# Kernel tuning notes

Hardware: AMD Instinct MI355X
Metric: run time of the kernel (lower is better)

Reference implementation:

```python
import jax, jax.numpy as jnp
import numpy as np

N_NODES = 50000
N_EDGES = 800000
F_IN, F_HID, F_OUT = 512, 64, 16


def setup_inputs() -> dict:
    key = jax.random.key(0)
    k1, k2, k3, k4, k5, k6 = jax.random.split(key, 6)
    x = jax.random.normal(k1, (N_NODES, F_IN), dtype=jnp.float32)
    edge_index = jax.random.randint(k2, (2, N_EDGES), 0, N_NODES, dtype=jnp.int64)
    # Glorot-style init for GCNConv linear weights, zero bias (PyG default)
    W1 = jax.random.normal(k3, (F_IN, F_HID), dtype=jnp.float32) * (1.0 / np.sqrt(F_IN))
    b1 = jnp.zeros((F_HID,), dtype=jnp.float32)
    W2 = jax.random.normal(k4, (F_HID, F_OUT), dtype=jnp.float32) * (1.0 / np.sqrt(F_HID))
    b2 = jnp.zeros((F_OUT,), dtype=jnp.float32)
    return {"x": x, "edge_index": edge_index, "W1": W1, "b1": b1, "W2": W2, "b2": b2}


def _gcn_conv(x, W, b, src, dst, norm, num_nodes):
    # x' = W x, then symmetric-normalized neighbor aggregation (scatter-add at dst)
    h = x @ W                                   # [N, F_out]
    msg = h[src] * norm[:, None]                # gather + scale  [E+N, F_out]
    out = jax.ops.segment_sum(msg, dst, num_segments=num_nodes)
    return out + b


def _gcn_norm(edge_index, num_nodes):
    # add self loops, compute deg^{-1/2}[src] * deg^{-1/2}[dst]
    loops = jnp.arange(num_nodes, dtype=edge_index.dtype)
    src = jnp.concatenate([edge_index[0], loops])
    dst = jnp.concatenate([edge_index[1], loops])
    deg = jax.ops.segment_sum(jnp.ones_like(dst, dtype=jnp.float32), dst,
                              num_segments=num_nodes)
    dinv = jnp.where(deg > 0, jax.lax.rsqrt(deg), 0.0)
    norm = dinv[src] * dinv[dst]                # [E+N]
    return src, dst, norm


def reference(x, edge_index, W1, b1, W2, b2):
    num_nodes = x.shape[0]
    src, dst, norm = _gcn_norm(edge_index, num_nodes)
    h = _gcn_conv(x, W1, b1, src, dst, norm, num_nodes)
    h = jax.nn.relu(h)
    return _gcn_conv(h, W2, b2, src, dst, norm, num_nodes)
```

## Files before the change

kernel.cpp:

```cpp
#include <hip/hip_runtime.h>

#define N_NODES 50000
#define N_EDGES 800000
#define F_IN    512
#define F_HID   64
#define F_OUT   16
#define NT      (N_NODES / 16)
#define GRID    512
#define CAP     64

typedef short bf16x8 __attribute__((ext_vector_type(8)));
typedef float f32x4  __attribute__((ext_vector_type(4)));

__device__ __forceinline__ short bhi_of(float v) {
    return (short)(__float_as_uint(v) >> 16);
}
__device__ __forceinline__ short blo_of(float v) {
    float hif = __uint_as_float(__float_as_uint(v) & 0xffff0000u);
    return (short)(__float_as_uint(v - hif) >> 16);
}

__global__ __launch_bounds__(512) void k_mega(const float* __restrict__ x,
                                              const float* __restrict__ W1,
                                              const int* __restrict__ src,
                                              const int* __restrict__ dst,
                                              int* __restrict__ count,
                                              int* __restrict__ padded,
                                              float* __restrict__ h) {
    for (int e = blockIdx.x * 512 + threadIdx.x; e < N_EDGES; e += GRID * 512) {
        int d = dst[e];
        int pos = atomicAdd(&count[d], 1);
        if (pos < CAP) padded[(size_t)d * CAP + pos] = src[e];
    }

    __shared__ __align__(16) float Abuf[2][8192];
    __shared__ float red[2][4][16][17];
    const int wave = threadIdx.x >> 6;
    const int lane = threadIdx.x & 63;
    const int m  = lane & 15, q = lane >> 4;
    const int kw = wave >> 2;
    const int cg = wave & 3;

    bf16x8 Bh[8], Bl[8];
#pragma unroll
    for (int s = 0; s < 8; ++s)
#pragma unroll
        for (int j = 0; j < 8; ++j) {
            float w = W1[(size_t)((kw * 8 + s) * 32 + q * 8 + j) * F_HID + cg * 16 + m];
            Bh[s][j] = bhi_of(w);
            Bl[s][j] = blo_of(w);
        }

    const int t0 = (int)(((long)NT * blockIdx.x) / GRID);
    const int t1 = (int)(((long)NT * (blockIdx.x + 1)) / GRID);

    int tile = t0;
    {
        const char* gb = (const char*)(x + (size_t)tile * 16 * F_IN);
        char* lb = (char*)&Abuf[0][0];
#pragma unroll
        for (int i = 0; i < 4; ++i) {
            const int c = wave * 4 + i;
            const int o = c * 1024 + lane * 16;
            const int sw = ((c >> 1) & 7) << 4;
            *(f32x4*)(lb + (o ^ sw)) = *(const f32x4*)(gb + o);
        }
    }
    __syncthreads();

    int p = 0;
    const int swr = (m & 7) << 4;
    while (true) {
        const int next = tile + 1;

        f32x4 v[4];
        if (next < t1) {
            const char* gb = (const char*)(x + (size_t)next * 16 * F_IN);
#pragma unroll
            for (int i = 0; i < 4; ++i) {
                const int o = (wave * 4 + i) * 1024 + lane * 16;
                v[i] = *(const f32x4*)(gb + o);
            }
        }

        f32x4 accA = {0, 0, 0, 0}, accB = {0, 0, 0, 0};
        const char* ab = (const char*)&Abuf[p][0];
#pragma unroll
        for (int s = 0; s < 8; ++s) {
            const int abase = m * 2048 + kw * 1024 + s * 128 + q * 32;
            f32x4 x0 = *(const f32x4*)(ab + (abase ^ swr));
            f32x4 x1 = *(const f32x4*)(ab + ((abase + 16) ^ swr));
            bf16x8 ahi, alo;
#pragma unroll
            for (int j = 0; j < 4; ++j) {
                ahi[j] = bhi_of(x0[j]);  alo[j] = blo_of(x0[j]);
                ahi[j + 4] = bhi_of(x1[j]);  alo[j + 4] = blo_of(x1[j]);
            }
            if (s & 1) {
                accB = __builtin_amdgcn_mfma_f32_16x16x32_bf16(ahi, Bh[s], accB, 0, 0, 0);
                accB = __builtin_amdgcn_mfma_f32_16x16x32_bf16(alo, Bh[s], accB, 0, 0, 0);
                accB = __builtin_amdgcn_mfma_f32_16x16x32_bf16(ahi, Bl[s], accB, 0, 0, 0);
            } else {
                accA = __builtin_amdgcn_mfma_f32_16x16x32_bf16(ahi, Bh[s], accA, 0, 0, 0);
                accA = __builtin_amdgcn_mfma_f32_16x16x32_bf16(alo, Bh[s], accA, 0, 0, 0);
                accA = __builtin_amdgcn_mfma_f32_16x16x32_bf16(ahi, Bl[s], accA, 0, 0, 0);
            }
        }
        f32x4 acc = accA + accB;

        if (next < t1) {
            char* lb = (char*)&Abuf[p ^ 1][0];
#pragma unroll
            for (int i = 0; i < 4; ++i) {
                const int c = wave * 4 + i;
                const int o = c * 1024 + lane * 16;
                const int sw = ((c >> 1) & 7) << 4;
                *(f32x4*)(lb + (o ^ sw)) = v[i];
            }
        }

        if (kw == 1) {
#pragma unroll
            for (int r = 0; r < 4; ++r)
                red[p][cg][q * 4 + r][m] = acc[r];
        }
        __syncthreads();

        if (kw == 0) {
            const int r0 = tile * 16;
#pragma unroll
            for (int r = 0; r < 4; ++r)
                h[(size_t)(r0 + q * 4 + r) * F_HID + cg * 16 + m] =
                    acc[r] + red[p][cg][q * 4 + r][m];
        }
        if (next >= t1) break;
        tile = next;
        p ^= 1;
    }
}

__global__ __launch_bounds__(256) void k_agg64f(const int* __restrict__ count,
                                                const int* __restrict__ padded,
                                                const float* __restrict__ h,
                                                const float* __restrict__ b1,
                                                const float* __restrict__ W2,
                                                float* __restrict__ h2,
                                                float* __restrict__ dinv) {
    __shared__ float h1s[4][65];
    __shared__ float W2s[64][17];
    for (int i = threadIdx.x; i < 64 * 16; i += 256)
        W2s[i >> 4][i & 15] = W2[i];

    const int wv = threadIdx.x >> 6;
    const int node = blockIdx.x * 4 + wv;
    const int j = threadIdx.x & 63;
    const int cnt = min(count[node], CAP);
    const float dn = rsqrtf((float)cnt + 1.0f);
    if (j == 0) dinv[node] = dn;
    const int* lst = padded + (size_t)node * CAP;

    float acc0 = h[(size_t)node * F_HID + j] * dn;
    float acc1 = 0.0f, acc2 = 0.0f, acc3 = 0.0f;
    int k = 0;
    for (; k + 8 <= cnt; k += 8) {
        int4 A = *(const int4*)(lst + k);
        int4 B = *(const int4*)(lst + k + 4);
        float w0 = rsqrtf((float)count[A.x] + 1.0f);
        float w1 = rsqrtf((float)count[A.y] + 1.0f);
        float w2 = rsqrtf((float)count[A.z] + 1.0f);
        float w3 = rsqrtf((float)count[A.w] + 1.0f);
        float w4 = rsqrtf((float)count[B.x] + 1.0f);
        float w5 = rsqrtf((float)count[B.y] + 1.0f);
        float w6 = rsqrtf((float)count[B.z] + 1.0f);
        float w7 = rsqrtf((float)count[B.w] + 1.0f);
        float v0 = h[(size_t)A.x * F_HID + j];
        float v1 = h[(size_t)A.y * F_HID + j];
        float v2 = h[(size_t)A.z * F_HID + j];
        float v3 = h[(size_t)A.w * F_HID + j];
        float v4 = h[(size_t)B.x * F_HID + j];
        float v5 = h[(size_t)B.y * F_HID + j];
        float v6 = h[(size_t)B.z * F_HID + j];
        float v7 = h[(size_t)B.w * F_HID + j];
        acc0 = fmaf(v0, w0, acc0);
        acc1 = fmaf(v1, w1, acc1);
        acc2 = fmaf(v2, w2, acc2);
        acc3 = fmaf(v3, w3, acc3);
        acc0 = fmaf(v4, w4, acc0);
        acc1 = fmaf(v5, w5, acc1);
        acc2 = fmaf(v6, w6, acc2);
        acc3 = fmaf(v7, w7, acc3);
    }
    for (; k < cnt; ++k) {
        int s = lst[k];
        acc0 = fmaf(h[(size_t)s * F_HID + j], rsqrtf((float)count[s] + 1.0f), acc0);
    }
    h1s[wv][j] = fmaxf(dn * ((acc0 + acc1) + (acc2 + acc3)) + b1[j], 0.0f);
    __syncthreads();

    const int oid  = threadIdx.x >> 2;
    const int part = threadIdx.x & 3;
    const int nd = oid >> 4, o = oid & 15;
    float s = 0.0f;
#pragma unroll
    for (int kk = 0; kk < 16; ++kk)
        s = fmaf(h1s[nd][part * 16 + kk], W2s[part * 16 + kk][o], s);
    s += __shfl_xor(s, 1);
    s += __shfl_xor(s, 2);
    if (part == 0)
        h2[(size_t)(blockIdx.x * 4 + nd) * F_OUT + o] = s;
}

__global__ __launch_bounds__(256) void k_agg16(const int* __restrict__ count,
                                               const int* __restrict__ padded,
                                               const float* __restrict__ dinv,
                                               const float* __restrict__ h2,
                                               const float* __restrict__ b2,
                                               float* __restrict__ out) {
    int node = blockIdx.x * 4 + (threadIdx.x >> 6);
    int lane = threadIdx.x & 63;
    int eo = lane >> 4;
    int j  = lane & 15;
    const int cnt = min(count[node], CAP);
    const float dn = dinv[node];
    const int* lst = padded + (size_t)node * CAP;
    float acc0 = 0.0f, acc1 = 0.0f, acc2 = 0.0f, acc3 = 0.0f;
    int k = eo;
    for (; k + 12 < cnt; k += 16) {
        int s0 = lst[k], s1 = lst[k + 4], s2 = lst[k + 8], s3 = lst[k + 12];
        float w0 = dinv[s0], w1 = dinv[s1], w2 = dinv[s2], w3 = dinv[s3];
        float v0 = h2[(size_t)s0 * F_OUT + j];
        float v1 = h2[(size_t)s1 * F_OUT + j];
        float v2 = h2[(size_t)s2 * F_OUT + j];
        float v3 = h2[(size_t)s3 * F_OUT + j];
        acc0 = fmaf(v0, w0, acc0);
        acc1 = fmaf(v1, w1, acc1);
        acc2 = fmaf(v2, w2, acc2);
        acc3 = fmaf(v3, w3, acc3);
    }
    for (; k < cnt; k += 4) {
        int s = lst[k];
        acc0 = fmaf(h2[(size_t)s * F_OUT + j], dinv[s], acc0);
    }
    float acc = (acc0 + acc1) + (acc2 + acc3);
    acc += __shfl_xor(acc, 16);
    acc += __shfl_xor(acc, 32);
    if (eo == 0)
        out[(size_t)node * F_OUT + j] =
            dn * (acc + dn * h2[(size_t)node * F_OUT + j]) + b2[j];
}

extern "C" void kernel_launch(void* const* d_in, const int* in_sizes, int n_in,
                              void* d_out, int out_size, void* d_ws, size_t ws_size,
                              hipStream_t stream) {
    const float* x  = (const float*)d_in[0];
    const int*   ei = (const int*)d_in[1];
    const float* W1 = (const float*)d_in[2];
    const float* b1 = (const float*)d_in[3];
    const float* W2 = (const float*)d_in[4];
    const float* b2 = (const float*)d_in[5];
    float* out = (float*)d_out;

    const int* src = ei;
    const int* dst = ei + N_EDGES;

    int* wsi = (int*)d_ws;
    int* count   = wsi;
    int* padded  = count + 50176;
    float* dinv  = (float*)(padded + (size_t)50176 * CAP);
    float* h     = dinv + 50176;
    float* h2    = h + (size_t)N_NODES * F_HID;

    (void)hipMemsetAsync(count, 0, 50176 * sizeof(int), stream);

    k_mega<<<GRID, 512, 0, stream>>>(x, W1, src, dst, count, padded, h);

    k_agg64f<<<N_NODES / 4, 256, 0, stream>>>(count, padded, h, b1, W2, h2, dinv);
    k_agg16<<<N_NODES / 4, 256, 0, stream>>>(count, padded, dinv, h2, b2, out);
}
```

Before: 285.4 us.

## Triple-buffer the x→h GEMM with direct global-to-LDS loads and a 4-way K split

Restructures the first-layer GEMM kernel to use 256 blocks of 1024 threads. The K dimension is split four ways across wave groups, and the old per-iteration register staging of x tiles is replaced with `global_load_lds` DMA into a triple-buffered LDS ring that prefetches two tiles ahead. Manual vmcnt waits and a single barrier per tile replace `__syncthreads`. A wider reduction buffer sums the four partial accumulators, and each wave writes one output row. The goal is to hide the x stream latency and free registers, at the cost of fragile hand-counted wait counters and more LDS per block.

```diff
diff --git a/kernel.cpp b/kernel.cpp
--- a/kernel.cpp
+++ b/kernel.cpp
@@ -6,7 +6,8 @@
 #define F_HID   64
 #define F_OUT   16
 #define NT      (N_NODES / 16)
-#define GRID    512
+#define GRIDM   256
+#define THREADS 1024
 #define CAP     64
 
 typedef short bf16x8 __attribute__((ext_vector_type(8)));
@@ -20,80 +21,92 @@
     return (short)(__float_as_uint(v - hif) >> 16);
 }
 
-__global__ __launch_bounds__(512) void k_mega(const float* __restrict__ x,
-                                              const float* __restrict__ W1,
-                                              const int* __restrict__ src,
-                                              const int* __restrict__ dst,
-                                              int* __restrict__ count,
-                                              int* __restrict__ padded,
-                                              float* __restrict__ h) {
-    for (int e = blockIdx.x * 512 + threadIdx.x; e < N_EDGES; e += GRID * 512) {
+__device__ __forceinline__ void gload16(const void* g, void* l) {
+    __builtin_amdgcn_global_load_lds(
+        (const __attribute__((address_space(1))) void*)g,
+        (__attribute__((address_space(3))) void*)l, 16, 0, 0);
+}
+
+__global__ __launch_bounds__(THREADS) void k_mega(const float* __restrict__ x,
+                                                  const float* __restrict__ W1,
+                                                  const int* __restrict__ src,
+                                                  const int* __restrict__ dst,
+                                                  int* __restrict__ count,
+                                                  int* __restrict__ padded,
+                                                  float* __restrict__ h) {
+    for (int e = blockIdx.x * THREADS + threadIdx.x; e < N_EDGES; e += GRIDM * THREADS) {
         int d = dst[e];
         int pos = atomicAdd(&count[d], 1);
         if (pos < CAP) padded[(size_t)d * CAP + pos] = src[e];
     }
 
-    __shared__ __align__(16) float Abuf[2][8192];
-    __shared__ float red[2][4][16][17];
-    const int wave = threadIdx.x >> 6;
+    __shared__ __align__(16) float Abuf[3][8192];
+    __shared__ float red[2][4][16][65];
+    const int wv   = threadIdx.x >> 6;
     const int lane = threadIdx.x & 63;
-    const int m  = lane & 15, q = lane >> 4;
-    const int kw = wave >> 2;
-    const int cg = wave & 3;
-
-    bf16x8 Bh[8], Bl[8];
-#pragma unroll
-    for (int s = 0; s < 8; ++s)
+    const int m = lane & 15, q = lane >> 4;
+    const int kw = wv >> 2;
+    const int cg = wv & 3;
+
+    bf16x8 Bh[4], Bl[4];
+#pragma unroll
+    for (int s = 0; s < 4; ++s)
 #pragma unroll
         for (int j = 0; j < 8; ++j) {
-            float w = W1[(size_t)((kw * 8 + s) * 32 + q * 8 + j) * F_HID + cg * 16 + m];
+            float w = W1[(size_t)(kw * 128 + s * 32 + q * 8 + j) * F_HID + cg * 16 + m];
             Bh[s][j] = bhi_of(w);
             Bl[s][j] = blo_of(w);
         }
 
-    const int t0 = (int)(((long)NT * blockIdx.x) / GRID);
-    const int t1 = (int)(((long)NT * (blockIdx.x + 1)) / GRID);
-
+    const int t0 = (int)(((long)NT * blockIdx.x) / GRIDM);
+    const int t1 = (int)(((long)NT * (blockIdx.x + 1)) / GRIDM);
+
+    const int c0 = wv * 2;
+    const int sw = (wv & 7) << 4;
+    const char* xb = (const char*)x;
+
+#pragma unroll
+    for (int i = 0; i < 2; ++i) {
+        const int c = c0 + i;
+        gload16(xb + (size_t)t0 * 32768 + c * 1024 + ((lane * 16) ^ sw),
+                (char*)&Abuf[0][0] + c * 1024);
+    }
+#pragma unroll
+    for (int i = 0; i < 2; ++i) {
+        const int c = c0 + i;
+        gload16(xb + (size_t)(t0 + 1) * 32768 + c * 1024 + ((lane * 16) ^ sw),
+                (char*)&Abuf[1][0] + c * 1024);
+    }
+    asm volatile("s_waitcnt vmcnt(2)" ::: "memory");
+    __builtin_amdgcn_sched_barrier(0);
+    __builtin_amdgcn_s_barrier();
+
+    const int swr = (m & 7) << 4;
     int tile = t0;
-    {
-        const char* gb = (const char*)(x + (size_t)tile * 16 * F_IN);
-        char* lb = (char*)&Abuf[0][0];
-#pragma unroll
-        for (int i = 0; i < 4; ++i) {
-            const int c = wave * 4 + i;
-            const int o = c * 1024 + lane * 16;
-            const int sw = ((c >> 1) & 7) << 4;
-            *(f32x4*)(lb + (o ^ sw)) = *(const f32x4*)(gb + o);
-        }
-    }
-    __syncthreads();
-
     int p = 0;
-    const int swr = (m & 7) << 4;
     while (true) {
-        const int next = tile + 1;
-
-        f32x4 v[4];
-        if (next < t1) {
-            const char* gb = (const char*)(x + (size_t)next * 16 * F_IN);
-#pragma unroll
-            for (int i = 0; i < 4; ++i) {
-                const int o = (wave * 4 + i) * 1024 + lane * 16;
-                v[i] = *(const f32x4*)(gb + o);
+        const int nx2 = tile + 2;
+        if (nx2 < t1) {
+            const char* gb = xb + (size_t)nx2 * 32768;
+            char* lb = (char*)&Abuf[(p + 2) % 3][0];
+#pragma unroll
+            for (int i = 0; i < 2; ++i) {
+                const int c = c0 + i;
+                gload16(gb + c * 1024 + ((lane * 16) ^ sw), lb + c * 1024);
             }
         }
 
         f32x4 accA = {0, 0, 0, 0}, accB = {0, 0, 0, 0};
         const char* ab = (const char*)&Abuf[p][0];
 #pragma unroll
-        for (int s = 0; s < 8; ++s) {
-            const int abase = m * 2048 + kw * 1024 + s * 128 + q * 32;
+        for (int s = 0; s < 4; ++s) {
+            const int abase = m * 2048 + kw * 512 + s * 128 + q * 32;
             f32x4 x0 = *(const f32x4*)(ab + (abase ^ swr));
             f32x4 x1 = *(const f32x4*)(ab + ((abase + 16) ^ swr));
             bf16x8 ahi, alo;
 #pragma unroll
             for (int j = 0; j < 4; ++j) {
-                ahi[j] = bhi_of(x0[j]);  alo[j] = blo_of(x0[j]);
+                ahi[j] = bhi_of(x0[j]);      alo[j] = blo_of(x0[j]);
                 ahi[j + 4] = bhi_of(x1[j]);  alo[j + 4] = blo_of(x1[j]);
             }
             if (s & 1) {
@@ -108,34 +121,28 @@
         }
         f32x4 acc = accA + accB;
 
-        if (next < t1) {
-            char* lb = (char*)&Abuf[p ^ 1][0];
-#pragma unroll
-            for (int i = 0; i < 4; ++i) {
-                const int c = wave * 4 + i;
-                const int o = c * 1024 + lane * 16;
-                const int sw = ((c >> 1) & 7) << 4;
-                *(f32x4*)(lb + (o ^ sw)) = v[i];
-            }
-        }
-
-        if (kw == 1) {
-#pragma unroll
-            for (int r = 0; r < 4; ++r)
-                red[p][cg][q * 4 + r][m] = acc[r];
-        }
-        __syncthreads();
-
-        if (kw == 0) {
-            const int r0 = tile * 16;
-#pragma unroll
-            for (int r = 0; r < 4; ++r)
-                h[(size_t)(r0 + q * 4 + r) * F_HID + cg * 16 + m] =
-                    acc[r] + red[p][cg][q * 4 + r][m];
-        }
-        if (next >= t1) break;
-        tile = next;
-        p ^= 1;
+        const int p2 = tile & 1;
+#pragma unroll
+        for (int r = 0; r < 4; ++r)
+            red[p2][kw][q * 4 + r][cg * 16 + m] = acc[r];
+
+        if (tile == t0) {
+            asm volatile("s_waitcnt vmcnt(2) lgkmcnt(0)" ::: "memory");
+        } else if (nx2 < t1) {
+            asm volatile("s_waitcnt vmcnt(3) lgkmcnt(0)" ::: "memory");
+        } else {
+            asm volatile("s_waitcnt vmcnt(1) lgkmcnt(0)" ::: "memory");
+        }
+        __builtin_amdgcn_sched_barrier(0);
+        __builtin_amdgcn_s_barrier();
+
+        float ssum = red[p2][0][wv][lane] + red[p2][1][wv][lane]
+                   + red[p2][2][wv][lane] + red[p2][3][wv][lane];
+        h[(size_t)(tile * 16 + wv) * F_HID + lane] = ssum;
+
+        if (tile + 1 >= t1) break;
+        tile += 1;
+        p = (p + 1) % 3;
     }
 }
 
@@ -272,7 +279,7 @@
 
     (void)hipMemsetAsync(count, 0, 50176 * sizeof(int), stream);
 
-    k_mega<<<GRID, 512, 0, stream>>>(x, W1, src, dst, count, padded, h);
+    k_mega<<<GRIDM, THREADS, 0, stream>>>(x, W1, src, dst, count, padded, h);
 
     k_agg64f<<<N_NODES / 4, 256, 0, stream>>>(count, padded, h, b1, W2, h2, dinv);
     k_agg16<<<N_NODES / 4, 256, 0, stream>>>(count, padded, dinv, h2, b2, out);
```

Result: slower. 304.4 us (+6.6%).

## Split edge-bucket build from GEMM and vectorize aggregation gathers per node

Applied to the files above, without the earlier changes.

Moves the edge bucketing out of the fused GEMM kernel into its own one-thread-per-edge kernel, which adds a launch but keeps the atomic scatter from delaying GEMM tiles. Both aggregation kernels now give each node a 16-lane (layer 1) or 4-lane (layer 2) group that gathers neighbour rows with float4 loads, so each wave covers several nodes and issues wider memory transactions. The second-layer projection in agg64f drops the shuffle reduction and has each thread do a 64-term dot product from shared memory.

```diff
diff --git a/kernel.cpp b/kernel.cpp
--- a/kernel.cpp
+++ b/kernel.cpp
@@ -20,19 +20,21 @@
     return (short)(__float_as_uint(v - hif) >> 16);
 }
 
-__global__ __launch_bounds__(512) void k_mega(const float* __restrict__ x,
-                                              const float* __restrict__ W1,
-                                              const int* __restrict__ src,
-                                              const int* __restrict__ dst,
-                                              int* __restrict__ count,
-                                              int* __restrict__ padded,
-                                              float* __restrict__ h) {
-    for (int e = blockIdx.x * 512 + threadIdx.x; e < N_EDGES; e += GRID * 512) {
+__global__ __launch_bounds__(256) void k_build(const int* __restrict__ src,
+                                               const int* __restrict__ dst,
+                                               int* __restrict__ count,
+                                               int* __restrict__ padded) {
+    int e = blockIdx.x * 256 + threadIdx.x;
+    if (e < N_EDGES) {
         int d = dst[e];
         int pos = atomicAdd(&count[d], 1);
         if (pos < CAP) padded[(size_t)d * CAP + pos] = src[e];
     }
-
+}
+
+__global__ __launch_bounds__(512) void k_gemm1(const float* __restrict__ x,
+                                               const float* __restrict__ W1,
+                                               float* __restrict__ h) {
     __shared__ __align__(16) float Abuf[2][8192];
     __shared__ float red[2][4][16][17];
     const int wave = threadIdx.x >> 6;
@@ -146,68 +148,59 @@
                                                 const float* __restrict__ W2,
                                                 float* __restrict__ h2,
                                                 float* __restrict__ dinv) {
-    __shared__ float h1s[4][65];
+    __shared__ float h1s[16][68];
     __shared__ float W2s[64][17];
     for (int i = threadIdx.x; i < 64 * 16; i += 256)
         W2s[i >> 4][i & 15] = W2[i];
 
-    const int wv = threadIdx.x >> 6;
-    const int node = blockIdx.x * 4 + wv;
-    const int j = threadIdx.x & 63;
-    const int cnt = min(count[node], CAP);
+    const int lane = threadIdx.x & 63;
+    const int wv   = threadIdx.x >> 6;
+    const int slot = lane >> 4;
+    const int fl   = lane & 15;
+    const int node = blockIdx.x * 16 + wv * 4 + slot;
+    const int cnt  = min(count[node], CAP);
     const float dn = rsqrtf((float)cnt + 1.0f);
-    if (j == 0) dinv[node] = dn;
+    if (fl == 0) dinv[node] = dn;
     const int* lst = padded + (size_t)node * CAP;
 
-    float acc0 = h[(size_t)node * F_HID + j] * dn;
-    float acc1 = 0.0f, acc2 = 0.0f, acc3 = 0.0f;
+    f32x4 accA = (*(const f32x4*)&h[(size_t)node * F_HID + fl * 4]) * dn;
+    f32x4 accB = {0, 0, 0, 0};
     int k = 0;
-    for (; k + 8 <= cnt; k += 8) {
-        int4 A = *(const int4*)(lst + k);
-        int4 B = *(const int4*)(lst + k + 4);
-        float w0 = rsqrtf((float)count[A.x] + 1.0f);
-        float w1 = rsqrtf((float)count[A.y] + 1.0f);
-        float w2 = rsqrtf((float)count[A.z] + 1.0f);
-        float w3 = rsqrtf((float)count[A.w] + 1.0f);
-        float w4 = rsqrtf((float)count[B.x] + 1.0f);
-        float w5 = rsqrtf((float)count[B.y] + 1.0f);
-        float w6 = rsqrtf((float)count[B.z] + 1.0f);
-        float w7 = rsqrtf((float)count[B.w] + 1.0f);
-        float v0 = h[(size_t)A.x * F_HID + j];
-        float v1 = h[(size_t)A.y * F_HID + j];
-        float v2 = h[(size_t)A.z * F_HID + j];
-        float v3 = h[(size_t)A.w * F_HID + j];
-        float v4 = h[(size_t)B.x * F_HID + j];
-        float v5 = h[(size_t)B.y * F_HID + j];
-        float v6 = h[(size_t)B.z * F_HID + j];
-        float v7 = h[(size_t)B.w * F_HID + j];
-        acc0 = fmaf(v0, w0, acc0);
-        acc1 = fmaf(v1, w1, acc1);
-        acc2 = fmaf(v2, w2, acc2);
-        acc3 = fmaf(v3, w3, acc3);
-        acc0 = fmaf(v4, w4, acc0);
-        acc1 = fmaf(v5, w5, acc1);
-        acc2 = fmaf(v6, w6, acc2);
-        acc3 = fmaf(v7, w7, acc3);
+    for (; k + 4 <= cnt; k += 4) {
+        int4 S = *(const int4*)(lst + k);
+        float w0 = rsqrtf((float)count[S.x] + 1.0f);
+        float w1 = rsqrtf((float)count[S.y] + 1.0f);
+        float w2 = rsqrtf((float)count[S.z] + 1.0f);
+        float w3 = rsqrtf((float)count[S.w] + 1.0f);
+        f32x4 v0 = *(const f32x4*)&h[(size_t)S.x * F_HID + fl * 4];
+        f32x4 v1 = *(const f32x4*)&h[(size_t)S.y * F_HID + fl * 4];
+        f32x4 v2 = *(const f32x4*)&h[(size_t)S.z * F_HID + fl * 4];
+        f32x4 v3 = *(const f32x4*)&h[(size_t)S.w * F_HID + fl * 4];
+        accA += v0 * w0;
+        accB += v1 * w1;
+        accA += v2 * w2;
+        accB += v3 * w3;
     }
     for (; k < cnt; ++k) {
         int s = lst[k];
-        acc0 = fmaf(h[(size_t)s * F_HID + j], rsqrtf((float)count[s] + 1.0f), acc0);
-    }
-    h1s[wv][j] = fmaxf(dn * ((acc0 + acc1) + (acc2 + acc3)) + b1[j], 0.0f);
+        accA += (*(const f32x4*)&h[(size_t)s * F_HID + fl * 4])
+              * rsqrtf((float)count[s] + 1.0f);
+    }
+    f32x4 r = (accA + accB) * dn;
+    const f32x4 bb = *(const f32x4*)&b1[fl * 4];
+    f32x4 h1v;
+#pragma unroll
+    for (int i = 0; i < 4; ++i)
+        h1v[i] = fmaxf(r[i] + bb[i], 0.0f);
+    *(f32x4*)&h1s[wv * 4 + slot][fl * 4] = h1v;
     __syncthreads();
 
-    const int oid  = threadIdx.x >> 2;
-    const int part = threadIdx.x & 3;
-    const int nd = oid >> 4, o = oid & 15;
+    const int nd = threadIdx.x >> 4, o = threadIdx.x & 15;
     float s = 0.0f;
 #pragma unroll
-    for (int kk = 0; kk < 16; ++kk)
-        s = fmaf(h1s[nd][part * 16 + kk], W2s[part * 16 + kk][o], s);
-    s += __shfl_xor(s, 1);
-    s += __shfl_xor(s, 2);
-    if (part == 0)
-        h2[(size_t)(blockIdx.x * 4 + nd) * F_OUT + o] = s;
+    for (int kk = 0; kk < 64; ++kk)
+        s = fmaf(h1s[nd][kk], W2s[kk][o], s);
+    h2[(size_t)(blockIdx.x * 16 + nd) * F_OUT + o] = s;
 }
 
 __global__ __launch_bounds__(256) void k_agg16(const int* __restrict__ count,
@@ -216,37 +209,38 @@
                                                const float* __restrict__ h2,
                                                const float* __restrict__ b2,
                                                float* __restrict__ out) {
-    int node = blockIdx.x * 4 + (threadIdx.x >> 6);
-    int lane = threadIdx.x & 63;
-    int eo = lane >> 4;
-    int j  = lane & 15;
-    const int cnt = min(count[node], CAP);
+    const int lane = threadIdx.x & 63;
+    const int wv   = threadIdx.x >> 6;
+    const int slot = lane >> 2;
+    const int fl   = lane & 3;
+    const int node = blockIdx.x * 64 + wv * 16 + slot;
+    if (node >= N_NODES) return;
+    const int cnt  = min(count[node], CAP);
     const float dn = dinv[node];
     const int* lst = padded + (size_t)node * CAP;
-    float acc0 = 0.0f, acc1 = 0.0f, acc2 = 0.0f, acc3 = 0.0f;
-    int k = eo;
-    for (; k + 12 < cnt; k += 16) {
-        int s0 = lst[k], s1 = lst[k + 4], s2 = lst[k + 8], s3 = lst[k + 12];
-        float w0 = dinv[s0], w1 = dinv[s1], w2 = dinv[s2], w3 = dinv[s3];
-        float v0 = h2[(size_t)s0 * F_OUT + j];
-        float v1 = h2[(size_t)s1 * F_OUT + j];
-        float v2 = h2[(size_t)s2 * F_OUT + j];
-        float v3 = h2[(size_t)s3 * F_OUT + j];
-        acc0 = fmaf(v0, w0, acc0);
-        acc1 = fmaf(v1, w1, acc1);
-        acc2 = fmaf(v2, w2, acc2);
-        acc3 = fmaf(v3, w3, acc3);
-    }
-    for (; k < cnt; k += 4) {
+
+    f32x4 accA = (*(const f32x4*)&h2[(size_t)node * F_OUT + fl * 4]) * dn;
+    f32x4 accB = {0, 0, 0, 0};
+    int k = 0;
+    for (; k + 4 <= cnt; k += 4) {
+        int4 S = *(const int4*)(lst + k);
+        float w0 = dinv[S.x], w1 = dinv[S.y], w2 = dinv[S.z], w3 = dinv[S.w];
+        f32x4 v0 = *(const f32x4*)&h2[(size_t)S.x * F_OUT + fl * 4];
+        f32x4 v1 = *(const f32x4*)&h2[(size_t)S.y * F_OUT + fl * 4];
+        f32x4 v2 = *(const f32x4*)&h2[(size_t)S.z * F_OUT + fl * 4];
+        f32x4 v3 = *(const f32x4*)&h2[(size_t)S.w * F_OUT + fl * 4];
+        accA += v0 * w0;
+        accB += v1 * w1;
+        accA += v2 * w2;
+        accB += v3 * w3;
+    }
+    for (; k < cnt; ++k) {
         int s = lst[k];
-        acc0 = fmaf(h2[(size_t)s * F_OUT + j], dinv[s], acc0);
-    }
-    float acc = (acc0 + acc1) + (acc2 + acc3);
-    acc += __shfl_xor(acc, 16);
-    acc += __shfl_xor(acc, 32);
-    if (eo == 0)
-        out[(size_t)node * F_OUT + j] =
-            dn * (acc + dn * h2[(size_t)node * F_OUT + j]) + b2[j];
+        accA += (*(const f32x4*)&h2[(size_t)s * F_OUT + fl * 4]) * dinv[s];
+    }
+    f32x4 r = (accA + accB) * dn;
+    const f32x4 bb = *(const f32x4*)&b2[fl * 4];
+    *(f32x4*)&out[(size_t)node * F_OUT + fl * 4] = r + bb;
 }
 
 extern "C" void kernel_launch(void* const* d_in, const int* in_sizes, int n_in,
@@ -272,8 +266,9 @@
 
     (void)hipMemsetAsync(count, 0, 50176 * sizeof(int), stream);
 
-    k_mega<<<GRID, 512, 0, stream>>>(x, W1, src, dst, count, padded, h);
-
-    k_agg64f<<<N_NODES / 4, 256, 0, stream>>>(count, padded, h, b1, W2, h2, dinv);
-    k_agg16<<<N_NODES / 4, 256, 0, stream>>>(count, padded, dinv, h2, b2, out);
-}
+    k_build<<<(N_EDGES + 255) / 256, 256, 0, stream>>>(src, dst, count, padded);
+    k_gemm1<<<GRID, 512, 0, stream>>>(x, W1, h);
+
+    k_agg64f<<<N_NODES / 16, 256, 0, stream>>>(count, padded, h, b1, W2, h2, dinv);
+    k_agg16<<<(N_NODES + 63) / 64, 256, 0, stream>>>(count, padded, dinv, h2, b2, out);
+}
```

Measured after the change: 266.7 us. 6.6% less time.
